# Kernel optimization log

Measured on AMD Instinct MI355X. Metric: run time of the kernel, lower is better.

Reference implementation:

```python
import jax, jax.numpy as jnp
import numpy as np

B, N, C, H = 1, 2048, 1024, 16


def setup_inputs() -> dict:
    key = jax.random.key(0)
    ks = jax.random.split(key, 8)
    scale = 1.0 / np.sqrt(C)
    d = {"x": jax.random.normal(ks[0], (B, N, C), dtype=jnp.float32)}
    for i, name in enumerate(["q1", "q2", "k1", "k2", "v", "out"]):
        d[f"W_{name}"] = jax.random.normal(ks[1 + i], (C, C), dtype=jnp.float32) * scale
        d[f"b_{name}"] = jnp.zeros((C,), dtype=jnp.float32)
    d["ln_g"] = jnp.ones((C,), dtype=jnp.float32)
    d["ln_b"] = jnp.zeros((C,), dtype=jnp.float32)
    return d


def reference(x, W_q1, b_q1, W_q2, b_q2, W_k1, b_k1, W_k2, b_k2,
              W_v, b_v, W_out, b_out, ln_g, ln_b):
    Bx, Nx, Cx = x.shape
    hd = Cx // H  # head_dim

    def proj(W, b):
        # ResidualMLP with num_layers=-1 and in_dim==out_dim: x + Linear(x)
        return x + x @ W + b

    def split_heads(z):
        return z.reshape(Bx, Nx, H, hd).transpose(0, 2, 1, 3)  # b h n d

    # kernel='identity', norm_q=norm_k=False -> raw projections
    q1 = split_heads(proj(W_q1, b_q1))
    q2 = split_heads(proj(W_q2, b_q2))
    k1 = split_heads(proj(W_k1, b_k1))
    k2 = split_heads(proj(W_k2, b_k2))
    v = split_heads(proj(W_v, b_v))

    # triple attention: elementwise product of the two Gram matrices, then
    # row-normalized (flash-style softmax; kernel also returns lse which the
    # module discards: `_, out = self.attn(...)`)
    s = jnp.einsum('bhnd,bhmd->bhnm', q1, k1) * jnp.einsum('bhnd,bhmd->bhnm', q2, k2)
    p = jax.nn.softmax(s, axis=-1)
    o = jnp.einsum('bhnm,bhmd->bhnd', p, v)

    o = o.transpose(0, 2, 1, 3).reshape(Bx, Nx, Cx)  # b n (h d)

    # LayerNorm (eps=1e-5, torch default)
    mu = o.mean(axis=-1, keepdims=True)
    var = ((o - mu) ** 2).mean(axis=-1, keepdims=True)
    o = (o - mu) / jnp.sqrt(var + 1e-5) * ln_g + ln_b

    return o @ W_out + b_out
```

## Files before the change

### kernel.cpp

```cpp
#include <hip/hip_runtime.h>
#include <hip/hip_bf16.h>
#include <stdint.h>


#define N_SEQ 2048
#define CDIM  1024
#define NHEAD 16
#define HDIM  64

typedef __attribute__((ext_vector_type(8))) short bfrag;
typedef __attribute__((ext_vector_type(4))) float f4;
typedef __attribute__((ext_vector_type(16))) float f16v;
typedef unsigned short u16;

#define MFMA16(a, b, c) __builtin_amdgcn_mfma_f32_16x16x32_bf16((a), (b), (c), 0, 0, 0)
#define MFMA32(a, b, c) __builtin_amdgcn_mfma_f32_32x32x16_bf16((a), (b), (c), 0, 0, 0)

__device__ __forceinline__ float bf2f(u16 u) {
  union { unsigned int i; float f; } c; c.i = ((unsigned int)u) << 16; return c.f;
}
__device__ __forceinline__ u16 f2bf(float f) {
  union { float f; unsigned int i; } c; c.f = f;
  unsigned int i = c.i;
  return (u16)((i + 0x7FFFu + ((i >> 16) & 1u)) >> 16);
}
__device__ __forceinline__ unsigned int pk2(float lo, float hi) {
  __hip_bfloat162 b = __float22bfloat162_rn(make_float2(lo, hi));
  unsigned int u;
  __builtin_memcpy(&u, &b, 4);
  return u;
}

__device__ __forceinline__ void gld16(const void* g, void* lds) {
  __builtin_amdgcn_global_load_lds(
      (const __attribute__((address_space(1))) void*)g,
      (__attribute__((address_space(3))) void*)lds, 16, 0, 0);
}

__global__ __launch_bounds__(256) void k_prep(
    const float* __restrict__ W0, const float* __restrict__ W1,
    const float* __restrict__ W2, const float* __restrict__ W3,
    const float* __restrict__ W4, const float* __restrict__ W5,
    const float* __restrict__ x,
    u16* __restrict__ wth, u16* __restrict__ wtl,
    u16* __restrict__ xh, u16* __restrict__ xl) {
  int wz = blockIdx.z;
  int t = threadIdx.x;
  if (wz >= 6) {
    int blk = (wz - 6) * 256 + blockIdx.y * 16 + blockIdx.x;
    int i = blk * 1024 + t * 4;
    float4 v = *(const float4*)(x + i);
    float vv[4] = {v.x, v.y, v.z, v.w};
    ushort4 h, l;
    u16 hh[4], ll[4];
#pragma unroll
    for (int j = 0; j < 4; j++) {
      hh[j] = f2bf(vv[j]);
      ll[j] = f2bf(vv[j] - bf2f(hh[j]));
    }
    h.x = hh[0]; h.y = hh[1]; h.z = hh[2]; h.w = hh[3];
    l.x = ll[0]; l.y = ll[1]; l.z = ll[2]; l.w = ll[3];
    *(ushort4*)(xh + i) = h;
    *(ushort4*)(xl + i) = l;
    return;
  }
  __shared__ float tile[64][65];
  const float* W = wz == 0 ? W0 : wz == 1 ? W1 : wz == 2 ? W2 : wz == 3 ? W3 : wz == 4 ? W4 : W5;
  int kb = blockIdx.x * 64, nb = blockIdx.y * 64;
  int r0 = t >> 4, c0 = (t & 15) * 4;
#pragma unroll
  for (int i = 0; i < 4; i++) {
    int r = r0 + i * 16;
    float4 v = *(const float4*)(W + (size_t)(kb + r) * CDIM + nb + c0);
    tile[r][c0 + 0] = v.x; tile[r][c0 + 1] = v.y; tile[r][c0 + 2] = v.z; tile[r][c0 + 3] = v.w;
  }
  __syncthreads();
#pragma unroll
  for (int i = 0; i < 4; i++) {
    int wn = (t >> 4) + i * 16;
    int wk = (t & 15) * 4;
    ushort4 h, l;
    u16 hh[4], ll[4];
#pragma unroll
    for (int j = 0; j < 4; j++) {
      float v = tile[wk + j][wn];
      hh[j] = f2bf(v);
      ll[j] = f2bf(v - bf2f(hh[j]));
    }
    h.x = hh[0]; h.y = hh[1]; h.z = hh[2]; h.w = hh[3];
    l.x = ll[0]; l.y = ll[1]; l.z = ll[2]; l.w = ll[3];
    size_t off = ((size_t)wz * CDIM + nb + wn) * CDIM + kb + wk;
    *(ushort4*)(wth + off) = h;
    if (wz < 4) *(ushort4*)(wtl + off) = l;
  }
}

__global__ __launch_bounds__(256, 2) void k_proj(
    const u16* __restrict__ xh, const u16* __restrict__ xl,
    const u16* __restrict__ wth, const u16* __restrict__ wtl,
    const float* __restrict__ x,
    const float* __restrict__ b0, const float* __restrict__ b1,
    const float* __restrict__ b2, const float* __restrict__ b3,
    const float* __restrict__ b4,
    u16* __restrict__ qh, u16* __restrict__ ql, u16* __restrict__ vT) {
  __shared__ u16 sAh[128 * 64];
  __shared__ u16 sAl[128 * 64];
  __shared__ u16 sBh[128 * 64];
  __shared__ u16 sBl[128 * 64];
  int t = threadIdx.x;
  int w = blockIdx.x >> 3;
  int n0 = (blockIdx.x & 7) * 128;
  int m0 = blockIdx.y * 128;
  int lane = t & 63, wid = t >> 6;
  int wm = (wid >> 1) * 64, wn = (wid & 1) * 64;
  int lr = lane & 15, lg = lane >> 4;
  const bool split = (w < 4);

  f4 acc[4][4];
#pragma unroll
  for (int i = 0; i < 4; i++)
#pragma unroll
    for (int j = 0; j < 4; j++) acc[i][j] = (f4)0.0f;

  const u16* wbh = wth + (size_t)w * CDIM * CDIM;
  const u16* wbl = wtl + (size_t)w * CDIM * CDIM;

  int srow = t >> 3;
  int scolsw = (((t & 7) ^ ((t >> 3) & 7)) * 8);
  int soff = srow * 64 + (t & 7) * 8;

  for (int kt = 0; kt < CDIM; kt += 64) {
#pragma unroll
    for (int c = 0; c < 4; c++) {
      gld16(xh + (size_t)(m0 + srow + c * 32) * CDIM + kt + scolsw, sAh + soff + c * 2048);
      gld16(wbh + (size_t)(n0 + srow + c * 32) * CDIM + kt + scolsw, sBh + soff + c * 2048);
      if (split) {
        gld16(xl + (size_t)(m0 + srow + c * 32) * CDIM + kt + scolsw, sAl + soff + c * 2048);
        gld16(wbl + (size_t)(n0 + srow + c * 32) * CDIM + kt + scolsw, sBl + soff + c * 2048);
      }
    }
    __syncthreads();
#pragma unroll
    for (int kk = 0; kk < 2; kk++) {
      int cc = (((kk * 4 + lg) ^ (lr & 7))) * 8;
      bfrag afh[4], bvh[4];
#pragma unroll
      for (int mi = 0; mi < 4; mi++)
        afh[mi] = *(const bfrag*)(sAh + (wm + mi * 16 + lr) * 64 + cc);
#pragma unroll
      for (int ni = 0; ni < 4; ni++)
        bvh[ni] = *(const bfrag*)(sBh + (wn + ni * 16 + lr) * 64 + cc);
#pragma unroll
      for (int mi = 0; mi < 4; mi++)
#pragma unroll
        for (int ni = 0; ni < 4; ni++)
          acc[mi][ni] = MFMA16(afh[mi], bvh[ni], acc[mi][ni]);
      if (split) {
        bfrag afl[4], bvl[4];
#pragma unroll
        for (int mi = 0; mi < 4; mi++)
          afl[mi] = *(const bfrag*)(sAl + (wm + mi * 16 + lr) * 64 + cc);
#pragma unroll
        for (int ni = 0; ni < 4; ni++)
          bvl[ni] = *(const bfrag*)(sBl + (wn + ni * 16 + lr) * 64 + cc);
#pragma unroll
        for (int mi = 0; mi < 4; mi++)
#pragma unroll
          for (int ni = 0; ni < 4; ni++) {
            acc[mi][ni] = MFMA16(afh[mi], bvl[ni], acc[mi][ni]);
            acc[mi][ni] = MFMA16(afl[mi], bvh[ni], acc[mi][ni]);
          }
      }
    }
    __syncthreads();
  }

  const float* bias = w == 0 ? b0 : w == 1 ? b1 : w == 2 ? b2 : w == 3 ? b3 : b4;
#pragma unroll
  for (int mi = 0; mi < 4; mi++) {
#pragma unroll
    for (int ni = 0; ni < 4; ni++) {
      int col = n0 + wn + ni * 16 + lr;
      int rowb = m0 + wm + mi * 16 + lg * 4;
      float vv[4];
#pragma unroll
      for (int r = 0; r < 4; r++)
        vv[r] = acc[mi][ni][r] + x[(size_t)(rowb + r) * CDIM + col] + bias[col];
      if (split) {
#pragma unroll
        for (int r = 0; r < 4; r++) {
          u16 h = f2bf(vv[r]);
          u16 l = f2bf(vv[r] - bf2f(h));
          qh[((size_t)w * N_SEQ + rowb + r) * CDIM + col] = h;
          ql[((size_t)w * N_SEQ + rowb + r) * CDIM + col] = l;
        }
      } else {
        ushort4 pv;
        pv.x = f2bf(vv[0]); pv.y = f2bf(vv[1]); pv.z = f2bf(vv[2]); pv.w = f2bf(vv[3]);
        *(ushort4*)(vT + (size_t)col * N_SEQ + rowb) = pv;
      }
    }
  }
}

__global__ __launch_bounds__(256, 2) void k_attn(
    const u16* __restrict__ qkh, const u16* __restrict__ qkl,
    const u16* __restrict__ vT, u16* __restrict__ O0, u16* __restrict__ O1,
    float2* __restrict__ ml) {
  __shared__ u16 sbuf[2][32 * 512];
  int bid = blockIdx.x;
  int khalf = bid >> 8;
  int inner = bid & 255;
  int vb = (inner & 7) * 32 + (inner >> 3);
  int h = vb >> 4;
  int qb = (vb & 15) * 128;
  int t = threadIdx.x, lane = t & 63, wv = t >> 6;
  int l31 = lane & 31, hi5 = lane >> 5;
  const size_t NC = (size_t)N_SEQ * CDIM;
  const int hoff = h * HDIM;
  const int k0 = khalf * (N_SEQ / 2);
  u16* Op = khalf ? O1 : O0;

  int qrow = qb + wv * 32 + l31;
  bfrag q1h[4], q1l[4], q2h[4], q2l[4];
#pragma unroll
  for (int ks = 0; ks < 4; ks++) {
    size_t off = (size_t)qrow * CDIM + hoff + ks * 16 + hi5 * 8;
    q1h[ks] = *(const bfrag*)(qkh + off);
    q1l[ks] = *(const bfrag*)(qkl + off);
    q2h[ks] = *(const bfrag*)(qkh + NC + off);
    q2l[ks] = *(const bfrag*)(qkl + NC + off);
  }

  const u16* kb = ((wv & 1) ? qkl : qkh) + (size_t)(2 + (wv >> 1)) * NC;

  float mrun = -1e30f, lrun = 0.f;
  f16v accO0 = (f16v)0.0f, accO1 = (f16v)0.0f;

#define STAGE(bi, kt)                                                          \
  {                                                                            \
    _Pragma("unroll") for (int i = 0; i < 8; i++) {                            \
      int kh_ = i >> 2, ksp_ = i & 3;                                          \
      gld16(kb + (size_t)((kt) + kh_ * 32 + l31) * CDIM + hoff + ksp_ * 16 +   \
                hi5 * 8,                                                       \
            sbuf[bi] + ((wv * 8 + i) << 9));                                   \
    }                                                                          \
  }

  STAGE(0, k0);
  asm volatile("s_waitcnt vmcnt(0)" ::: "memory");
  __builtin_amdgcn_s_barrier();

#pragma unroll 1
  for (int it = 0; it < N_SEQ / 2 / 64; it++) {
    int kt = k0 + it * 64;
    if (it + 1 < N_SEQ / 2 / 64) STAGE((it + 1) & 1, kt + 64);

    bfrag vld[2][4];
#pragma unroll
    for (int kh = 0; kh < 2; kh++) {
      const u16* vb0 = vT + (size_t)(hoff + l31) * N_SEQ + kt + kh * 32 + hi5 * 8;
      const u16* vb1 = vT + (size_t)(hoff + 32 + l31) * N_SEQ + kt + kh * 32 + hi5 * 8;
      vld[kh][0] = *(const bfrag*)(vb0);
      vld[kh][1] = *(const bfrag*)(vb0 + 16);
      vld[kh][2] = *(const bfrag*)(vb1);
      vld[kh][3] = *(const bfrag*)(vb1 + 16);
    }

    const u16* sb = sbuf[it & 1];
    f16v s1[2], s2[2];
#pragma unroll
    for (int kh = 0; kh < 2; kh++) { s1[kh] = (f16v)0.0f; s2[kh] = (f16v)0.0f; }
#pragma unroll
    for (int kh = 0; kh < 2; kh++) {
#pragma unroll
      for (int ks = 0; ks < 4; ks++) {
        const u16* cb = sb + ((kh * 4 + ks) << 9) + lane * 8;
        bfrag k1h = *(const bfrag*)(cb);
        bfrag k1l = *(const bfrag*)(cb + (8 << 9));
        bfrag k2h = *(const bfrag*)(cb + (16 << 9));
        bfrag k2l = *(const bfrag*)(cb + (24 << 9));
        s1[kh] = MFMA32(k1h, q1h[ks], s1[kh]);
        s1[kh] = MFMA32(k1h, q1l[ks], s1[kh]);
        s1[kh] = MFMA32(k1l, q1h[ks], s1[kh]);
        s2[kh] = MFMA32(k2h, q2h[ks], s2[kh]);
        s2[kh] = MFMA32(k2h, q2l[ks], s2[kh]);
        s2[kh] = MFMA32(k2l, q2h[ks], s2[kh]);
      }
    }
    f16v p0 = s1[0] * s2[0];
    f16v p1 = s1[1] * s2[1];

    float pm = fmaxf(p0[0], p1[0]);
#pragma unroll
    for (int j = 1; j < 16; j++) pm = fmaxf(pm, fmaxf(p0[j], p1[j]));
    pm = fmaxf(pm, __shfl_xor(pm, 32, 64));
    if (__any(pm > mrun + 8.0f)) {
      float mnew = fmaxf(mrun, pm);
      float sc = __expf(mrun - mnew);
      lrun *= sc;
#pragma unroll
      for (int j = 0; j < 16; j++) { accO0[j] *= sc; accO1[j] *= sc; }
      mrun = mnew;
    }
    float rs = 0.f;
#pragma unroll
    for (int j = 0; j < 16; j++) { p0[j] = __expf(p0[j] - mrun); rs += p0[j]; }
#pragma unroll
    for (int j = 0; j < 16; j++) { p1[j] = __expf(p1[j] - mrun); rs += p1[j]; }
    rs += __shfl_xor(rs, 32, 64);
    lrun += rs;

    unsigned dw[16];
#pragma unroll
    for (int j = 0; j < 8; j++) dw[j] = pk2(p0[2 * j], p0[2 * j + 1]);
#pragma unroll
    for (int j = 0; j < 8; j++) dw[8 + j] = pk2(p1[2 * j], p1[2 * j + 1]);

#pragma unroll
    for (int kh = 0; kh < 2; kh++) {
      unsigned j0 = dw[kh * 8 + 0], j1 = dw[kh * 8 + 1], j2 = dw[kh * 8 + 2],
               j3 = dw[kh * 8 + 3], j4 = dw[kh * 8 + 4], j5 = dw[kh * 8 + 5],
               j6 = dw[kh * 8 + 6], j7 = dw[kh * 8 + 7];
      unsigned pj0 = __shfl_xor(j0, 32, 64), pj1 = __shfl_xor(j1, 32, 64);
      unsigned pj2 = __shfl_xor(j2, 32, 64), pj3 = __shfl_xor(j3, 32, 64);
      unsigned pj4 = __shfl_xor(j4, 32, 64), pj5 = __shfl_xor(j5, 32, 64);
      unsigned pj6 = __shfl_xor(j6, 32, 64), pj7 = __shfl_xor(j7, 32, 64);
      union { unsigned u[4]; bfrag b; } f0, f1;
      f0.u[0] = hi5 ? pj2 : j0;
      f0.u[1] = hi5 ? pj3 : j1;
      f0.u[2] = hi5 ? j2 : pj0;
      f0.u[3] = hi5 ? j3 : pj1;
      f1.u[0] = hi5 ? pj6 : j4;
      f1.u[1] = hi5 ? pj7 : j5;
      f1.u[2] = hi5 ? j6 : pj4;
      f1.u[3] = hi5 ? j7 : pj5;
      accO0 = MFMA32(vld[kh][0], f0.b, accO0);
      accO0 = MFMA32(vld[kh][1], f1.b, accO0);
      accO1 = MFMA32(vld[kh][2], f0.b, accO1);
      accO1 = MFMA32(vld[kh][3], f1.b, accO1);
    }

    asm volatile("s_waitcnt vmcnt(0)" ::: "memory");
    __builtin_amdgcn_s_barrier();
  }
#undef STAGE

#pragma unroll
  for (int q4 = 0; q4 < 4; q4++) {
    ushort4 s0, s1v;
    s0.x = f2bf(accO0[q4 * 4 + 0]); s0.y = f2bf(accO0[q4 * 4 + 1]);
    s0.z = f2bf(accO0[q4 * 4 + 2]); s0.w = f2bf(accO0[q4 * 4 + 3]);
    s1v.x = f2bf(accO1[q4 * 4 + 0]); s1v.y = f2bf(accO1[q4 * 4 + 1]);
    s1v.z = f2bf(accO1[q4 * 4 + 2]); s1v.w = f2bf(accO1[q4 * 4 + 3]);
    *(ushort4*)(Op + (size_t)qrow * CDIM + hoff + q4 * 8 + hi5 * 4) = s0;
    *(ushort4*)(Op + (size_t)qrow * CDIM + hoff + 32 + q4 * 8 + hi5 * 4) = s1v;
  }
  if (!hi5) ml[(size_t)(khalf * NHEAD + h) * N_SEQ + qrow] = make_float2(mrun, lrun);
}

__global__ __launch_bounds__(256) void k_cln(
    const u16* __restrict__ O0, const u16* __restrict__ O1,
    const float2* __restrict__ ml, const float* __restrict__ g,
    const float* __restrict__ b, u16* __restrict__ oln) {
  __shared__ float rsm[4], rs2m[4];
  int row = blockIdx.x, t = threadIdx.x;
  int h = t >> 4;
  float2 a = ml[(size_t)h * N_SEQ + row];
  float2 bb = ml[(size_t)(NHEAD + h) * N_SEQ + row];
  float M = fmaxf(a.x, bb.x);
  float w0 = __expf(a.x - M), w1 = __expf(bb.x - M);
  float invL = 1.0f / (w0 * a.y + w1 * bb.y);
  ushort4 u0 = *(const ushort4*)(O0 + (size_t)row * CDIM + t * 4);
  ushort4 u1 = *(const ushort4*)(O1 + (size_t)row * CDIM + t * 4);
  float vals[4];
  vals[0] = (w0 * bf2f(u0.x) + w1 * bf2f(u1.x)) * invL;
  vals[1] = (w0 * bf2f(u0.y) + w1 * bf2f(u1.y)) * invL;
  vals[2] = (w0 * bf2f(u0.z) + w1 * bf2f(u1.z)) * invL;
  vals[3] = (w0 * bf2f(u0.w) + w1 * bf2f(u1.w)) * invL;
  float s = vals[0] + vals[1] + vals[2] + vals[3];
  float s2 = vals[0] * vals[0] + vals[1] * vals[1] + vals[2] * vals[2] + vals[3] * vals[3];
#pragma unroll
  for (int d = 1; d < 64; d <<= 1) {
    s += __shfl_xor(s, d, 64);
    s2 += __shfl_xor(s2, d, 64);
  }
  int wv = t >> 6;
  if ((t & 63) == 0) { rsm[wv] = s; rs2m[wv] = s2; }
  __syncthreads();
  s = rsm[0] + rsm[1] + rsm[2] + rsm[3];
  s2 = rs2m[0] + rs2m[1] + rs2m[2] + rs2m[3];
  float mu = s * (1.0f / CDIM);
  float var = s2 * (1.0f / CDIM) - mu * mu;
  float inv = rsqrtf(var + 1e-5f);
  ushort4 r4;
  u16 rr[4];
#pragma unroll
  for (int j = 0; j < 4; j++) {
    int col = t * 4 + j;
    rr[j] = f2bf((vals[j] - mu) * inv * g[col] + b[col]);
  }
  r4.x = rr[0]; r4.y = rr[1]; r4.z = rr[2]; r4.w = rr[3];
  *(ushort4*)(oln + (size_t)row * CDIM + t * 4) = r4;
}

__global__ __launch_bounds__(256, 2) void k_ogemm(
    const u16* __restrict__ A, const u16* __restrict__ Bw,
    const float* __restrict__ bias, float* __restrict__ out) {
  __shared__ u16 sA[64 * 64];
  __shared__ u16 sB[128 * 64];
  int t = threadIdx.x;
  int n0 = blockIdx.x * 128, m0 = blockIdx.y * 64;
  int lane = t & 63, wid = t >> 6;
  int wm = (wid >> 1) * 32, wn = (wid & 1) * 64;
  int lr = lane & 15, lg = lane >> 4;
  f4 acc[2][4];
#pragma unroll
  for (int i = 0; i < 2; i++)
#pragma unroll
    for (int j = 0; j < 4; j++) acc[i][j] = (f4)0.0f;
  int srow = t >> 3, scol = (t & 7) * 8, soff = srow * 64 + scol;
  for (int kt = 0; kt < CDIM; kt += 64) {
#pragma unroll
    for (int c = 0; c < 2; c++)
      gld16(A + (size_t)(m0 + srow + c * 32) * CDIM + kt + scol, (u16*)sA + soff + c * 2048);
#pragma unroll
    for (int c = 0; c < 4; c++)
      gld16(Bw + (size_t)(n0 + srow + c * 32) * CDIM + kt + scol, (u16*)sB + soff + c * 2048);
    __syncthreads();
#pragma unroll
    for (int kk = 0; kk < 2; kk++) {
      bfrag af[2], bv[4];
#pragma unroll
      for (int mi = 0; mi < 2; mi++)
        af[mi] = *(const bfrag*)(sA + (wm + mi * 16 + lr) * 64 + kk * 32 + lg * 8);
#pragma unroll
      for (int ni = 0; ni < 4; ni++)
        bv[ni] = *(const bfrag*)(sB + (wn + ni * 16 + lr) * 64 + kk * 32 + lg * 8);
#pragma unroll
      for (int mi = 0; mi < 2; mi++)
#pragma unroll
        for (int ni = 0; ni < 4; ni++)
          acc[mi][ni] = MFMA16(af[mi], bv[ni], acc[mi][ni]);
    }
    __syncthreads();
  }
#pragma unroll
  for (int mi = 0; mi < 2; mi++) {
#pragma unroll
    for (int ni = 0; ni < 4; ni++) {
      int col = n0 + wn + ni * 16 + lr;
      int rowb = m0 + wm + mi * 16 + lg * 4;
#pragma unroll
      for (int r = 0; r < 4; r++)
        out[(size_t)(rowb + r) * CDIM + col] = acc[mi][ni][r] + bias[col];
    }
  }
}

extern "C" void kernel_launch(void* const* d_in, const int* in_sizes, int n_in,
                              void* d_out, int out_size, void* d_ws, size_t ws_size,
                              hipStream_t stream) {
  const float* x   = (const float*)d_in[0];
  const float* Wq1 = (const float*)d_in[1];  const float* bq1 = (const float*)d_in[2];
  const float* Wq2 = (const float*)d_in[3];  const float* bq2 = (const float*)d_in[4];
  const float* Wk1 = (const float*)d_in[5];  const float* bk1 = (const float*)d_in[6];
  const float* Wk2 = (const float*)d_in[7];  const float* bk2 = (const float*)d_in[8];
  const float* Wv  = (const float*)d_in[9];  const float* bv  = (const float*)d_in[10];
  const float* Wo  = (const float*)d_in[11]; const float* bo  = (const float*)d_in[12];
  const float* lng = (const float*)d_in[13]; const float* lnb = (const float*)d_in[14];

  char* w = (char*)d_ws;
  u16* xh  = (u16*)(w + (0ull << 20));
  u16* xl  = (u16*)(w + (4ull << 20));
  u16* wth = (u16*)(w + (8ull << 20));
  u16* wtl = (u16*)(w + (20ull << 20));
  u16* qsh = (u16*)(w + (28ull << 20));
  u16* qsl = (u16*)(w + (44ull << 20));
  u16* vT  = (u16*)(w + (60ull << 20));
  u16* O0  = (u16*)(w + (0ull << 20));
  u16* O1  = (u16*)(w + (4ull << 20));
  float2* ml = (float2*)(w + (20ull << 20));
  u16* oln = (u16*)(w + (24ull << 20));

  k_prep<<<dim3(16, 16, 14), 256, 0, stream>>>(Wq1, Wq2, Wk1, Wk2, Wv, Wo, x,
                                               wth, wtl, xh, xl);
  k_proj<<<dim3(40, 16), 256, 0, stream>>>(xh, xl, wth, wtl, x,
                                           bq1, bq2, bk1, bk2, bv, qsh, qsl, vT);
  k_attn<<<512, 256, 0, stream>>>(qsh, qsl, vT, O0, O1, ml);
  k_cln<<<2048, 256, 0, stream>>>(O0, O1, ml, lng, lnb, oln);
  k_ogemm<<<dim3(8, 32), 256, 0, stream>>>(oln, wth + 5ull * CDIM * CDIM, bo, (float*)d_out);
}
```

Measured before the change: 186.2 us.

## Double-buffer projection GEMM shared-memory tiles with K=32 prefetch pipeline

The projection GEMM now uses two shared-memory buffers with a K-step of 32. It prefetches the next tile with direct-to-LDS loads while computing on the current one, and waits with an explicit vmcnt and barrier. A new paired-row swizzled layout keeps LDS reads conflict-free at the narrower K width. The aim is to hide global load latency behind MFMA work, at the cost of twice as many loop iterations and barriers.

Measured after the change: 193.3 us. +3.8%, slower.

```diff
diff --git a/kernel.cpp b/kernel.cpp
--- a/kernel.cpp
+++ b/kernel.cpp
@@ -103,10 +103,7 @@
     const float* __restrict__ b2, const float* __restrict__ b3,
     const float* __restrict__ b4,
     u16* __restrict__ qh, u16* __restrict__ ql, u16* __restrict__ vT) {
-  __shared__ u16 sAh[128 * 64];
-  __shared__ u16 sAl[128 * 64];
-  __shared__ u16 sBh[128 * 64];
-  __shared__ u16 sBl[128 * 64];
+  __shared__ u16 sbuf[2][4][64 * 64];
   int t = threadIdx.x;
   int w = blockIdx.x >> 3;
   int n0 = (blockIdx.x & 7) * 128;
@@ -125,55 +122,78 @@
   const u16* wbh = wth + (size_t)w * CDIM * CDIM;
   const u16* wbl = wtl + (size_t)w * CDIM * CDIM;
 
-  int srow = t >> 3;
-  int scolsw = (((t & 7) ^ ((t >> 3) & 7)) * 8);
-  int soff = srow * 64 + (t & 7) * 8;
-
-  for (int kt = 0; kt < CDIM; kt += 64) {
-#pragma unroll
-    for (int c = 0; c < 4; c++) {
-      gld16(xh + (size_t)(m0 + srow + c * 32) * CDIM + kt + scolsw, sAh + soff + c * 2048);
-      gld16(wbh + (size_t)(n0 + srow + c * 32) * CDIM + kt + scolsw, sBh + soff + c * 2048);
-      if (split) {
-        gld16(xl + (size_t)(m0 + srow + c * 32) * CDIM + kt + scolsw, sAl + soff + c * 2048);
-        gld16(wbl + (size_t)(n0 + srow + c * 32) * CDIM + kt + scolsw, sBl + soff + c * 2048);
-      }
-    }
-    __syncthreads();
-#pragma unroll
-    for (int kk = 0; kk < 2; kk++) {
-      int cc = (((kk * 4 + lg) ^ (lr & 7))) * 8;
-      bfrag afh[4], bvh[4];
+  int rS[2], cS[2], qS[2];
+#pragma unroll
+  for (int p = 0; p < 2; p++) {
+    int q_ = t + p * 256;
+    int R_ = q_ >> 3, s_ = q_ & 7;
+    int cp_ = s_ ^ (R_ & 7);
+    rS[p] = 2 * R_ + (cp_ >> 2);
+    cS[p] = (cp_ & 3) * 8;
+    qS[p] = q_ * 8;
+  }
+
+#define STAGEP(bi, kt)                                                        \
+  {                                                                           \
+    _Pragma("unroll") for (int p = 0; p < 2; p++) {                           \
+      size_t ga_ = (size_t)(m0 + rS[p]) * CDIM + (kt) + cS[p];                \
+      size_t gb_ = (size_t)(n0 + rS[p]) * CDIM + (kt) + cS[p];                \
+      gld16(xh + ga_, &sbuf[bi][0][qS[p]]);                                   \
+      gld16(wbh + gb_, &sbuf[bi][2][qS[p]]);                                  \
+      if (split) {                                                            \
+        gld16(xl + ga_, &sbuf[bi][1][qS[p]]);                                 \
+        gld16(wbl + gb_, &sbuf[bi][3][qS[p]]);                                \
+      }                                                                       \
+    }                                                                         \
+  }
+
+  int offA[4], offB[4];
+#pragma unroll
+  for (int i = 0; i < 4; i++) {
+    int ra = wm + i * 16 + lr;
+    offA[i] = (ra >> 1) * 64 + (((((ra & 1) << 2) | lg) ^ ((ra >> 1) & 7)) * 8);
+    int rb = wn + i * 16 + lr;
+    offB[i] = (rb >> 1) * 64 + (((((rb & 1) << 2) | lg) ^ ((rb >> 1) & 7)) * 8);
+  }
+
+  STAGEP(0, 0);
+  asm volatile("s_waitcnt vmcnt(0)" ::: "memory");
+  __builtin_amdgcn_s_barrier();
+
+#pragma unroll 1
+  for (int it = 0; it < CDIM / 32; it++) {
+    int cb = it & 1;
+    if (it + 1 < CDIM / 32) STAGEP(cb ^ 1, (it + 1) * 32);
+
+    bfrag afh[4], bvh[4];
+#pragma unroll
+    for (int mi = 0; mi < 4; mi++) afh[mi] = *(const bfrag*)(&sbuf[cb][0][offA[mi]]);
+#pragma unroll
+    for (int ni = 0; ni < 4; ni++) bvh[ni] = *(const bfrag*)(&sbuf[cb][2][offB[ni]]);
+#pragma unroll
+    for (int mi = 0; mi < 4; mi++)
+#pragma unroll
+      for (int ni = 0; ni < 4; ni++)
+        acc[mi][ni] = MFMA16(afh[mi], bvh[ni], acc[mi][ni]);
+    if (split) {
+      bfrag afl[4], bvl[4];
+#pragma unroll
+      for (int mi = 0; mi < 4; mi++) afl[mi] = *(const bfrag*)(&sbuf[cb][1][offA[mi]]);
+#pragma unroll
+      for (int ni = 0; ni < 4; ni++) bvl[ni] = *(const bfrag*)(&sbuf[cb][3][offB[ni]]);
 #pragma unroll
       for (int mi = 0; mi < 4; mi++)
-        afh[mi] = *(const bfrag*)(sAh + (wm + mi * 16 + lr) * 64 + cc);
-#pragma unroll
-      for (int ni = 0; ni < 4; ni++)
-        bvh[ni] = *(const bfrag*)(sBh + (wn + ni * 16 + lr) * 64 + cc);
-#pragma unroll
-      for (int mi = 0; mi < 4; mi++)
-#pragma unroll
-        for (int ni = 0; ni < 4; ni++)
-          acc[mi][ni] = MFMA16(afh[mi], bvh[ni], acc[mi][ni]);
-      if (split) {
-        bfrag afl[4], bvl[4];
-#pragma unroll
-        for (int mi = 0; mi < 4; mi++)
-          afl[mi] = *(const bfrag*)(sAl + (wm + mi * 16 + lr) * 64 + cc);
-#pragma unroll
-        for (int ni = 0; ni < 4; ni++)
-          bvl[ni] = *(const bfrag*)(sBl + (wn + ni * 16 + lr) * 64 + cc);
-#pragma unroll
-        for (int mi = 0; mi < 4; mi++)
-#pragma unroll
-          for (int ni = 0; ni < 4; ni++) {
-            acc[mi][ni] = MFMA16(afh[mi], bvl[ni], acc[mi][ni]);
-            acc[mi][ni] = MFMA16(afl[mi], bvh[ni], acc[mi][ni]);
-          }
-      }
-    }
-    __syncthreads();
-  }
+#pragma unroll
+        for (int ni = 0; ni < 4; ni++) {
+          acc[mi][ni] = MFMA16(afh[mi], bvl[ni], acc[mi][ni]);
+          acc[mi][ni] = MFMA16(afl[mi], bvh[ni], acc[mi][ni]);
+        }
+    }
+
+    asm volatile("s_waitcnt vmcnt(0)" ::: "memory");
+    __builtin_amdgcn_s_barrier();
+  }
+#undef STAGEP
 
   const float* bias = w == 0 ? b0 : w == 1 ? b1 : w == 2 ? b2 : w == 3 ? b3 : b4;
 #pragma unroll
```
